# Kernel tuning notes

Measured on AMD Instinct MI355X. Metric: run time of the kernel, lower is better.

## Reference

```python
import jax, jax.numpy as jnp
import numpy as np

N = 100000   # nodes
E = 800000   # edges
D = 64       # hidden_channels
H = 4        # heads
C = D        # out_channels per head (PyG: out_channels=hidden)


def setup_inputs() -> dict:
    key = jax.random.key(0)
    ks = jax.random.split(key, 20)
    inp = {}
    inp['x'] = jax.random.normal(ks[0], (N, D), dtype=jnp.float32)
    inp['edge_index'] = jax.random.randint(ks[1], (2, E), 0, N, dtype=jnp.int32)
    i = 2
    for layer in (1, 2):
        for nm in ('Wq', 'Wk', 'Wv'):
            inp[f'{nm}{layer}'] = jax.random.normal(ks[i], (D, H * C), dtype=jnp.float32) * 0.05; i += 1
            inp[f'b{nm[1]}{layer}'] = jnp.zeros((H * C,), dtype=jnp.float32)
        inp[f'Ws{layer}'] = jax.random.normal(ks[i], (D, D), dtype=jnp.float32) * 0.05; i += 1
        inp[f'bs{layer}'] = jnp.zeros((D,), dtype=jnp.float32)
    return inp


def _transformer_conv(x, src, dst, Wq, bq, Wk, bk, Wv, bv, Ws, bs):
    n = x.shape[0]
    q = (x @ Wq + bq).reshape(n, H, C)
    k = (x @ Wk + bk).reshape(n, H, C)
    v = (x @ Wv + bv).reshape(n, H, C)
    # per-edge attention logits: [E, H]
    alpha = jnp.einsum('ehc,ehc->eh', q[dst], k[src]) / np.sqrt(C).astype(np.float32)
    # segment softmax over incoming edges of each destination node
    amax = jax.ops.segment_max(alpha, dst, num_segments=n)          # [N, H]
    ex = jnp.exp(alpha - amax[dst])                                 # [E, H]
    denom = jax.ops.segment_sum(ex, dst, num_segments=n)           # [N, H]
    attn = ex / (denom[dst] + 1e-16)                                # [E, H]
    msg = v[src] * attn[:, :, None]                                 # [E, H, C]
    agg = jax.ops.segment_sum(msg, dst, num_segments=n)            # [N, H, C]
    # concat=False -> mean over heads; root_weight skip connection
    return agg.mean(axis=1) + x @ Ws + bs


def reference(x, edge_index, Wq1, bq1, Wk1, bk1, Wv1, bv1, Ws1, bs1,
              Wq2, bq2, Wk2, bk2, Wv2, bv2, Ws2, bs2):
    src, dst = edge_index[0], edge_index[1]
    h = _transformer_conv(x, src, dst, Wq1, bq1, Wk1, bk1, Wv1, bv1, Ws1, bs1)
    h = jax.nn.relu(h)
    out = _transformer_conv(h, src, dst, Wq2, bq2, Wk2, bk2, Wv2, bv2, Ws2, bs2)
    return out
```

## Files before the change

kernel.cpp:

```cpp
#include <hip/hip_runtime.h>
#include <hip/hip_fp16.h>
#include <math.h>


typedef __attribute__((ext_vector_type(8))) short bf16x8;
typedef __attribute__((ext_vector_type(4))) float f32x4;
typedef __attribute__((ext_vector_type(2))) float f32x2;

#define QKSCALE 32.0f
#define C_EXP2 1.760325e-4f

__device__ inline unsigned short f2bf(float f) {
    unsigned int u = __float_as_uint(f);
    u = (u + 0x7fffu + ((u >> 16) & 1u)) >> 16;
    return (unsigned short)u;
}

#if __has_builtin(__builtin_amdgcn_cvt_pk_fp8_f32) && __has_builtin(__builtin_amdgcn_cvt_pk_f32_fp8)
#define HW_FP8 1
#endif

#ifndef HW_FP8
__device__ inline unsigned int fp8_enc1(float f) {
    unsigned int u = __float_as_uint(f);
    unsigned int s = (u >> 24) & 0x80u;
    float a = fabsf(f);
    if (a >= 448.f) return s | 0x7Eu;
    if (a < 0.015625f) return s;
    unsigned int ua = __float_as_uint(a);
    unsigned int r = ua + 0x7FFFFu + ((ua >> 20) & 1u);
    int e = (int)((r >> 23) & 255u) - 120;
    unsigned int m = (r >> 20) & 7u;
    if (e < 1) return s;
    if (e > 15) return s | 0x7Eu;
    return s | (unsigned int)((e << 3) | m);
}
__device__ inline float fp8_dec1(unsigned int b) {
    unsigned int e = (b >> 3) & 15u, m = b & 7u;
    float v;
    if (e) v = __uint_as_float(((e + 120u) << 23) | (m << 20));
    else   v = (float)m * 0.001953125f;
    return (b & 0x80u) ? -v : v;
}
#endif

__device__ inline unsigned int fp8x4_pack(float f0, float f1, float f2, float f3) {
#ifdef HW_FP8
    int pk = __builtin_amdgcn_cvt_pk_fp8_f32(f0, f1, 0, false);
    pk = __builtin_amdgcn_cvt_pk_fp8_f32(f2, f3, pk, true);
    return (unsigned int)pk;
#else
    return fp8_enc1(f0) | (fp8_enc1(f1) << 8) | (fp8_enc1(f2) << 16) | (fp8_enc1(f3) << 24);
#endif
}

__device__ inline float4 fp8x4_unpack(unsigned int k) {
#ifdef HW_FP8
    f32x2 lo = __builtin_amdgcn_cvt_pk_f32_fp8((int)k, false);
    f32x2 hi = __builtin_amdgcn_cvt_pk_f32_fp8((int)k, true);
    return make_float4(lo[0], lo[1], hi[0], hi[1]);
#else
    return make_float4(fp8_dec1(k & 255u), fp8_dec1((k >> 8) & 255u),
                       fp8_dec1((k >> 16) & 255u), fp8_dec1(k >> 24));
#endif
}

__device__ inline unsigned int i8x4_pack(float f0, float f1, float f2, float f3) {
    int a = (int)rintf(f0 * QKSCALE); a = a < -127 ? -127 : (a > 127 ? 127 : a);
    int b = (int)rintf(f1 * QKSCALE); b = b < -127 ? -127 : (b > 127 ? 127 : b);
    int c = (int)rintf(f2 * QKSCALE); c = c < -127 ? -127 : (c > 127 ? 127 : c);
    int d = (int)rintf(f3 * QKSCALE); d = d < -127 ? -127 : (d > 127 ? 127 : d);
    return (unsigned int)((a & 255) | ((b & 255) << 8) | ((c & 255) << 16) | ((d & 255) << 24));
}

__device__ inline int sdot4(unsigned int a, unsigned int b, int c) {
#if __has_builtin(__builtin_amdgcn_sdot4)
    return __builtin_amdgcn_sdot4((int)a, (int)b, c, false);
#else
    int r = c;
#pragma unroll
    for (int i = 0; i < 4; ++i) {
        int ai = (int)(a << (24 - 8 * i)) >> 24;
        int bi = (int)(b << (24 - 8 * i)) >> 24;
        r += ai * bi;
    }
    return r;
#endif
}

__global__ void k_setup(
    const float* __restrict__ x, unsigned short* __restrict__ Xb, int ncast4,
    const float* __restrict__ Wq1, const float* __restrict__ Wk1,
    const float* __restrict__ Wv1, const float* __restrict__ Ws1,
    const float* __restrict__ Wq2, const float* __restrict__ Wk2,
    const float* __restrict__ Wv2, const float* __restrict__ Ws2,
    unsigned short* __restrict__ Wt,
    int* __restrict__ counts, int N, int castBl)
{
    int b = blockIdx.x, tid = threadIdx.x;
    if (b < castBl) {
        int i = b * 256 + tid;
        if (i < ncast4) {
            float4 v = ((const float4*)x)[i];
            ushort4 o;
            o.x = f2bf(v.x); o.y = f2bf(v.y); o.z = f2bf(v.z); o.w = f2bf(v.w);
            ((ushort4*)Xb)[i] = o;
        }
    } else if (b < castBl + 416) {
        int j = (b - castBl) * 256 + tid;
        int layer = j / 53248;
        int r = j % 53248;
        if (r < 49152) {
            int m = r / 16384, w = r % 16384;
            int n = w / 64, k = w % 64;
            const float* W = (layer == 0)
                ? ((m == 0) ? Wq1 : (m == 1) ? Wk1 : Wv1)
                : ((m == 0) ? Wq2 : (m == 1) ? Wk2 : Wv2);
            Wt[layer * 53248 + m * 16384 + n * 64 + k] = f2bf(W[k * 256 + n]);
        } else {
            int w = r - 49152;
            int n = w / 64, k = w % 64;
            const float* W = (layer == 0) ? Ws1 : Ws2;
            Wt[layer * 53248 + 49152 + n * 64 + k] = f2bf(W[k * 64 + n]);
        }
    } else {
        int i = (b - castBl - 416) * 256 + tid;
        if (i < N) counts[i] = 0;
    }
}

#define SCAN_B 256
#define SCAN_CHUNK 2048
__global__ void k_scan1(const int* __restrict__ counts, int n,
                        int* __restrict__ offs, int* __restrict__ bsums) {
    __shared__ int lds[SCAN_B];
    int b = blockIdx.x, tid = threadIdx.x;
    int base = b * SCAN_CHUNK + tid * 8;
    int v[8]; int s = 0;
#pragma unroll
    for (int i = 0; i < 8; ++i) { int idx = base + i; int c = (idx < n) ? counts[idx] : 0; v[i] = s; s += c; }
    lds[tid] = s;
    for (int off = 1; off < SCAN_B; off <<= 1) {
        __syncthreads();
        int x = (tid >= off) ? lds[tid - off] : 0;
        __syncthreads();
        lds[tid] += x;
    }
    __syncthreads();
    int texcl = lds[tid] - s;
#pragma unroll
    for (int i = 0; i < 8; ++i) { int idx = base + i; if (idx < n) offs[idx] = texcl + v[i]; }
    if (tid == SCAN_B - 1) bsums[b] = lds[tid];
}

__global__ void k_scan2(int* bsums, int nb) {
    __shared__ int lds[256];
    int t = threadIdx.x;
    if (nb > 256) {
        if (t == 0) { int s = 0; for (int i = 0; i < nb; ++i) { int c = bsums[i]; bsums[i] = s; s += c; } }
        return;
    }
    int v = (t < nb) ? bsums[t] : 0;
    lds[t] = v;
    for (int off = 1; off < 256; off <<= 1) {
        __syncthreads();
        int x = (t >= off) ? lds[t - off] : 0;
        __syncthreads();
        lds[t] += x;
    }
    __syncthreads();
    if (t < nb) bsums[t] = lds[t] - v;
}

__global__ void k_scatter(const int* __restrict__ src, const int* __restrict__ dst, int E,
                          const int* __restrict__ offs, const int* __restrict__ bsums,
                          const int* __restrict__ rank, int* __restrict__ csr_src) {
    int e = blockIdx.x * 256 + threadIdx.x;
    if (e < E) {
        int d = dst[e];
        csr_src[offs[d] + bsums[d >> 11] + rank[e]] = src[e];
    }
}

#define GST 68
__global__ __launch_bounds__(256) void k_gemm(
    const unsigned short* __restrict__ Xb, int nrows,
    const unsigned short* __restrict__ WtL,
    const float* __restrict__ bqp, const float* __restrict__ bkp,
    const float* __restrict__ bvp, const float* __restrict__ bsp,
    unsigned char* __restrict__ Qb, unsigned char* __restrict__ KVb,
    unsigned char* __restrict__ Sb,
    const int* __restrict__ dstp, int histE,
    int* __restrict__ counts, int* __restrict__ rank, int gemmBl)
{
    __shared__ unsigned char st[4 * 64 * GST];
    int tid = threadIdx.x;
    if (blockIdx.x >= gemmBl) {
        int e = (blockIdx.x - gemmBl) * 256 + tid;
        if (e < histE) rank[e] = atomicAdd(&counts[dstp[e]], 1);
        return;
    }
    int wave = tid >> 6, lane = tid & 63;
    int quad = lane >> 4, n16 = lane & 15;
    int r0 = blockIdx.x * 64;
    unsigned char* wst = st + wave * 64 * GST;

    const unsigned short* Wq = WtL;
    const unsigned short* Wk = WtL + 16384;
    const unsigned short* Wv = WtL + 32768;
    const unsigned short* Ws = WtL + 49152;

    bf16x8 fQ[8], fK[8], fV[8], fS[2];
    float4 cQ[4], cK[4], cV[4], cS;
#pragma unroll
    for (int c = 0; c < 4; ++c) {
        int ct = wave * 4 + c;
        int roff = (ct * 16 + n16) * 64 + quad * 8;
        fQ[2 * c]     = *(const bf16x8*)(Wq + roff);
        fQ[2 * c + 1] = *(const bf16x8*)(Wq + roff + 32);
        fK[2 * c]     = *(const bf16x8*)(Wk + roff);
        fK[2 * c + 1] = *(const bf16x8*)(Wk + roff + 32);
        fV[2 * c]     = *(const bf16x8*)(Wv + roff);
        fV[2 * c + 1] = *(const bf16x8*)(Wv + roff + 32);
        cQ[c] = *(const float4*)(bqp + ct * 16 + quad * 4);
        cK[c] = *(const float4*)(bkp + ct * 16 + quad * 4);
        cV[c] = *(const float4*)(bvp + ct * 16 + quad * 4);
    }
    {
        int roff = (wave * 16 + n16) * 64 + quad * 8;
        fS[0] = *(const bf16x8*)(Ws + roff);
        fS[1] = *(const bf16x8*)(Ws + roff + 32);
        cS = *(const float4*)(bsp + wave * 16 + quad * 4);
    }
    bf16x8 a0[4], a1[4];
#pragma unroll
    for (int g = 0; g < 4; ++g) {
        int node = r0 + g * 16 + n16;
        int nodec = (node < nrows) ? node : (nrows - 1);
        a0[g] = *(const bf16x8*)(Xb + (size_t)nodec * 64 + quad * 8);
        a1[g] = *(const bf16x8*)(Xb + (size_t)nodec * 64 + 32 + quad * 8);
    }

    auto do_mat = [&](const bf16x8* fm, const float4* cm,
                      unsigned char* base, int stride, bool isInt8) {
#pragma unroll
        for (int g = 0; g < 4; ++g) {
#pragma unroll
            for (int c = 0; c < 4; ++c) {
                f32x4 acc = {0.f, 0.f, 0.f, 0.f};
                acc = __builtin_amdgcn_mfma_f32_16x16x32_bf16(fm[2 * c], a0[g], acc, 0, 0, 0);
                acc = __builtin_amdgcn_mfma_f32_16x16x32_bf16(fm[2 * c + 1], a1[g], acc, 0, 0, 0);
                float f0 = acc[0] + cm[c].x, f1 = acc[1] + cm[c].y;
                float f2 = acc[2] + cm[c].z, f3 = acc[3] + cm[c].w;
                unsigned int pk = isInt8 ? i8x4_pack(f0, f1, f2, f3)
                                         : fp8x4_pack(f0, f1, f2, f3);
                *(unsigned int*)(wst + (g * 16 + n16) * GST + c * 16 + quad * 4) = pk;
            }
        }
#pragma unroll
        for (int it = 0; it < 4; ++it) {
            int row = it * 16 + (lane >> 2);
            uint4 v = *(const uint4*)(wst + row * GST + (lane & 3) * 16);
            int node = r0 + row;
            if (node < nrows)
                *(uint4*)(base + (size_t)node * stride + wave * 64 + (lane & 3) * 16) = v;
        }
    };
    do_mat(fQ, cQ, Qb, 256, true);
    do_mat(fK, cK, KVb, 512, true);
    do_mat(fV, cV, KVb + 256, 512, false);
#pragma unroll
    for (int g = 0; g < 4; ++g) {
        f32x4 acc = {0.f, 0.f, 0.f, 0.f};
        acc = __builtin_amdgcn_mfma_f32_16x16x32_bf16(fS[0], a0[g], acc, 0, 0, 0);
        acc = __builtin_amdgcn_mfma_f32_16x16x32_bf16(fS[1], a1[g], acc, 0, 0, 0);
        *(float4*)(wst + (g * 16 + n16) * GST + quad * 16) =
            make_float4(acc[0] + cS.x, acc[1] + cS.y, acc[2] + cS.z, acc[3] + cS.w);
    }
#pragma unroll
    for (int it = 0; it < 4; ++it) {
        int row = it * 16 + (lane >> 2);
        uint4 v = *(const uint4*)(wst + row * GST + (lane & 3) * 16);
        int node = r0 + row;
        if (node < nrows)
            *(uint4*)(Sb + (size_t)node * 256 + wave * 64 + (lane & 3) * 16) = v;
    }
}

__global__ __launch_bounds__(256) void k_attn(
    const unsigned char* __restrict__ Qb, const unsigned char* __restrict__ KVb,
    const unsigned char* __restrict__ Sb,
    const int* __restrict__ offs, const int* __restrict__ bsums,
    const int* __restrict__ csr_src,
    float* __restrict__ out, unsigned short* __restrict__ Xb,
    int n, int Etot, int mode)
{
    int node = blockIdx.x * 4 + (threadIdx.x >> 6);
    if (node >= n) return;
    int lane = threadIdx.x & 63;
    int sl = lane & 31;
    int half = lane >> 5;
    uint2 q8 = *(const uint2*)(Qb + (size_t)node * 256 + sl * 8);
    int beg = offs[node] + bsums[node >> 11];
    int end = (node + 1 < n) ? (offs[node + 1] + bsums[(node + 1) >> 11]) : Etot;
    float l = 0.f;
    float acc[8];
#pragma unroll
    for (int i = 0; i < 8; ++i) acc[i] = 0.f;
    for (int base = beg; base < end; base += 8) {
        int cnt = end - base; if (cnt > 8) cnt = 8;
        int my = (lane < cnt) ? csr_src[base + lane] : 0;
        uint2 kk[4], vv[4];
#pragma unroll
        for (int p = 0; p < 4; ++p) {
            int idx = __shfl(my, 2 * p + half);
            const unsigned char* row = KVb + (size_t)idx * 512 + sl * 8;
            kk[p] = *(const uint2*)(row);
            vv[p] = *(const uint2*)(row + 256);
        }
#pragma unroll
        for (int p = 0; p < 4; ++p) {
            int d = sdot4(kk[p].x, q8.x, 0);
            d = sdot4(kk[p].y, q8.y, d);
            d += __shfl_xor(d, 1); d += __shfl_xor(d, 2); d += __shfl_xor(d, 4);
            float w = __builtin_exp2f((float)d * C_EXP2);
            w = (2 * p + half < cnt) ? w : 0.f;
            l += w;
            float4 va = fp8x4_unpack(vv[p].x);
            float4 vb = fp8x4_unpack(vv[p].y);
            acc[0] += va.x * w; acc[1] += va.y * w;
            acc[2] += va.z * w; acc[3] += va.w * w;
            acc[4] += vb.x * w; acc[5] += vb.y * w;
            acc[6] += vb.z * w; acc[7] += vb.w * w;
        }
    }
    l += __shfl_xor(l, 32);
#pragma unroll
    for (int i = 0; i < 8; ++i) acc[i] += __shfl_xor(acc[i], 32);
    float inv = 1.f / (l + 1e-16f);
#pragma unroll
    for (int i = 0; i < 8; ++i) acc[i] *= inv;
#pragma unroll
    for (int i = 0; i < 8; ++i) {
        acc[i] += __shfl_xor(acc[i], 8);
        acc[i] += __shfl_xor(acc[i], 16);
        acc[i] *= 0.25f;
    }
    if (lane < 8) {
        const float* Srow = (const float*)(Sb + (size_t)node * 256);
        float4 s0 = *(const float4*)(Srow + lane * 8);
        float4 s1 = *(const float4*)(Srow + lane * 8 + 4);
        float r0 = acc[0] + s0.x, r1 = acc[1] + s0.y;
        float r2 = acc[2] + s0.z, r3 = acc[3] + s0.w;
        float r4 = acc[4] + s1.x, r5 = acc[5] + s1.y;
        float r6 = acc[6] + s1.z, r7 = acc[7] + s1.w;
        if (mode == 1) {
            r0 = fmaxf(r0, 0.f); r1 = fmaxf(r1, 0.f);
            r2 = fmaxf(r2, 0.f); r3 = fmaxf(r3, 0.f);
            r4 = fmaxf(r4, 0.f); r5 = fmaxf(r5, 0.f);
            r6 = fmaxf(r6, 0.f); r7 = fmaxf(r7, 0.f);
            uint4 o;
            o.x = (unsigned int)f2bf(r0) | ((unsigned int)f2bf(r1) << 16);
            o.y = (unsigned int)f2bf(r2) | ((unsigned int)f2bf(r3) << 16);
            o.z = (unsigned int)f2bf(r4) | ((unsigned int)f2bf(r5) << 16);
            o.w = (unsigned int)f2bf(r6) | ((unsigned int)f2bf(r7) << 16);
            *(uint4*)(Xb + (size_t)node * 64 + lane * 8) = o;
        } else {
            *(float4*)(out + (size_t)node * 64 + lane * 8) = make_float4(r0, r1, r2, r3);
            *(float4*)(out + (size_t)node * 64 + lane * 8 + 4) = make_float4(r4, r5, r6, r7);
        }
    }
}

extern "C" void kernel_launch(void* const* d_in, const int* in_sizes, int n_in,
                              void* d_out, int out_size, void* d_ws, size_t ws_size,
                              hipStream_t stream)
{
    const float* x  = (const float*)d_in[0];
    const int*   ei = (const int*)d_in[1];
    int N = in_sizes[0] / 64;
    int E = in_sizes[1] / 2;
    const int* srcp = ei;
    const int* dstp = ei + E;
    const float* Wq1 = (const float*)d_in[2],  *bq1 = (const float*)d_in[3];
    const float* Wk1 = (const float*)d_in[4],  *bk1 = (const float*)d_in[5];
    const float* Wv1 = (const float*)d_in[6],  *bv1 = (const float*)d_in[7];
    const float* Ws1 = (const float*)d_in[8],  *bs1 = (const float*)d_in[9];
    const float* Wq2 = (const float*)d_in[10], *bq2 = (const float*)d_in[11];
    const float* Wk2 = (const float*)d_in[12], *bk2 = (const float*)d_in[13];
    const float* Wv2 = (const float*)d_in[14], *bv2 = (const float*)d_in[15];
    const float* Ws2 = (const float*)d_in[16], *bs2 = (const float*)d_in[17];
    float* out = (float*)d_out;

    char* ws = (char*)d_ws;
    size_t off = 0;
    auto alloc = [&](size_t bytes) -> void* {
        void* p = ws + off;
        off = (off + bytes + 255) & ~(size_t)255;
        return p;
    };
    unsigned short* Xb = (unsigned short*)alloc((size_t)N * 64 * 2);
    unsigned char* Qb  = (unsigned char*)alloc(((size_t)N + 64) * 256);
    unsigned char* KVb = (unsigned char*)alloc(((size_t)N + 64) * 512);
    unsigned char* Sb  = (unsigned char*)alloc(((size_t)N + 64) * 256);
    unsigned short* Wt = (unsigned short*)alloc(2 * 53248 * 2);
    int* counts = (int*)alloc((size_t)N * 4);
    int* rank   = (int*)alloc((size_t)E * 4);
    int* offs   = (int*)alloc((size_t)N * 4);
    int* bsums  = (int*)alloc(1024 * 4);
    int* csr    = (int*)alloc((size_t)E * 4);
    (void)n_in; (void)out_size;
    if (off > ws_size) return;

    int ebl = (E + 255) / 256;
    int nb_scan = (N + SCAN_CHUNK - 1) / SCAN_CHUNK;
    int row_bl = (N + 63) / 64;
    int attn_bl = (N + 3) / 4;
    int ncast4 = N * 16;
    int castBl = (ncast4 + 255) / 256;
    int zeroBl = (N + 255) / 256;

    k_setup<<<castBl + 416 + zeroBl, 256, 0, stream>>>(
        x, Xb, ncast4, Wq1, Wk1, Wv1, Ws1, Wq2, Wk2, Wv2, Ws2, Wt, counts, N, castBl);

    k_gemm<<<row_bl + ebl, 256, 0, stream>>>(
        Xb, N, Wt, bq1, bk1, bv1, bs1, Qb, KVb, Sb,
        dstp, E, counts, rank, row_bl);

    k_scan1<<<nb_scan, SCAN_B, 0, stream>>>(counts, N, offs, bsums);
    k_scan2<<<1, 256, 0, stream>>>(bsums, nb_scan);
    k_scatter<<<ebl, 256, 0, stream>>>(srcp, dstp, E, offs, bsums, rank, csr);

    k_attn<<<attn_bl, 256, 0, stream>>>(Qb, KVb, Sb, offs, bsums, csr, out, Xb, N, E, 1);

    k_gemm<<<row_bl, 256, 0, stream>>>(
        Xb, N, Wt + 53248, bq2, bk2, bv2, bs2, Qb, KVb, Sb,
        dstp, 0, counts, rank, row_bl);

    k_attn<<<attn_bl, 256, 0, stream>>>(Qb, KVb, Sb, offs, bsums, csr, out, Xb, N, E, 0);
}
```

Before: 405.3 us.

## Interleave per-node Q/K/V/S into one 1KB record and double-buffer GEMM staging

Merges the separate Q, KV and S buffers into one per-node 1024-byte record (Q, K, V, S at fixed offsets). The GEMM now stages full 64-row tiles across all waves in two LDS buffers and writes whole contiguous rows, so stores are more coalesced. Weight loading is now per matrix, which reduces register pressure and allows a launch_bounds occupancy hint of 4. The cost is block-wide syncs between stages, plus a wider 1KB stride for the gathered K/V rows in attention, which may hurt cache-line locality for those gathers.

```diff
diff --git a/kernel.cpp b/kernel.cpp
--- a/kernel.cpp
+++ b/kernel.cpp
@@ -182,18 +182,17 @@
     }
 }
 
-#define GST 68
-__global__ __launch_bounds__(256) void k_gemm(
+#define GROW 272
+__global__ __launch_bounds__(256, 4) void k_gemm(
     const unsigned short* __restrict__ Xb, int nrows,
     const unsigned short* __restrict__ WtL,
     const float* __restrict__ bqp, const float* __restrict__ bkp,
     const float* __restrict__ bvp, const float* __restrict__ bsp,
-    unsigned char* __restrict__ Qb, unsigned char* __restrict__ KVb,
-    unsigned char* __restrict__ Sb,
+    unsigned char* __restrict__ NB,
     const int* __restrict__ dstp, int histE,
     int* __restrict__ counts, int* __restrict__ rank, int gemmBl)
 {
-    __shared__ unsigned char st[4 * 64 * GST];
+    __shared__ unsigned char st[2][64 * GROW];
     int tid = threadIdx.x;
     if (blockIdx.x >= gemmBl) {
         int e = (blockIdx.x - gemmBl) * 256 + tid;
@@ -203,35 +202,7 @@
     int wave = tid >> 6, lane = tid & 63;
     int quad = lane >> 4, n16 = lane & 15;
     int r0 = blockIdx.x * 64;
-    unsigned char* wst = st + wave * 64 * GST;
-
-    const unsigned short* Wq = WtL;
-    const unsigned short* Wk = WtL + 16384;
-    const unsigned short* Wv = WtL + 32768;
-    const unsigned short* Ws = WtL + 49152;
-
-    bf16x8 fQ[8], fK[8], fV[8], fS[2];
-    float4 cQ[4], cK[4], cV[4], cS;
-#pragma unroll
-    for (int c = 0; c < 4; ++c) {
-        int ct = wave * 4 + c;
-        int roff = (ct * 16 + n16) * 64 + quad * 8;
-        fQ[2 * c]     = *(const bf16x8*)(Wq + roff);
-        fQ[2 * c + 1] = *(const bf16x8*)(Wq + roff + 32);
-        fK[2 * c]     = *(const bf16x8*)(Wk + roff);
-        fK[2 * c + 1] = *(const bf16x8*)(Wk + roff + 32);
-        fV[2 * c]     = *(const bf16x8*)(Wv + roff);
-        fV[2 * c + 1] = *(const bf16x8*)(Wv + roff + 32);
-        cQ[c] = *(const float4*)(bqp + ct * 16 + quad * 4);
-        cK[c] = *(const float4*)(bkp + ct * 16 + quad * 4);
-        cV[c] = *(const float4*)(bvp + ct * 16 + quad * 4);
-    }
-    {
-        int roff = (wave * 16 + n16) * 64 + quad * 8;
-        fS[0] = *(const bf16x8*)(Ws + roff);
-        fS[1] = *(const bf16x8*)(Ws + roff + 32);
-        cS = *(const float4*)(bsp + wave * 16 + quad * 4);
-    }
+
     bf16x8 a0[4], a1[4];
 #pragma unroll
     for (int g = 0; g < 4; ++g) {
@@ -241,55 +212,84 @@
         a1[g] = *(const bf16x8*)(Xb + (size_t)nodec * 64 + 32 + quad * 8);
     }
 
-    auto do_mat = [&](const bf16x8* fm, const float4* cm,
-                      unsigned char* base, int stride, bool isInt8) {
-#pragma unroll
-        for (int g = 0; g < 4; ++g) {
-#pragma unroll
-            for (int c = 0; c < 4; ++c) {
+    bf16x8 f[8]; float4 cb[4];
+    auto loadW = [&](const unsigned short* W, const float* bp) {
+#pragma unroll
+        for (int c = 0; c < 4; ++c) {
+            int roff = ((wave * 4 + c) * 16 + n16) * 64 + quad * 8;
+            f[2 * c]     = *(const bf16x8*)(W + roff);
+            f[2 * c + 1] = *(const bf16x8*)(W + roff + 32);
+            cb[c]        = *(const float4*)(bp + (wave * 4 + c) * 16 + quad * 4);
+        }
+    };
+    auto stage = [&](int buf, bool isInt8) {
+#pragma unroll
+        for (int c = 0; c < 4; ++c) {
+#pragma unroll
+            for (int g = 0; g < 4; ++g) {
                 f32x4 acc = {0.f, 0.f, 0.f, 0.f};
-                acc = __builtin_amdgcn_mfma_f32_16x16x32_bf16(fm[2 * c], a0[g], acc, 0, 0, 0);
-                acc = __builtin_amdgcn_mfma_f32_16x16x32_bf16(fm[2 * c + 1], a1[g], acc, 0, 0, 0);
-                float f0 = acc[0] + cm[c].x, f1 = acc[1] + cm[c].y;
-                float f2 = acc[2] + cm[c].z, f3 = acc[3] + cm[c].w;
+                acc = __builtin_amdgcn_mfma_f32_16x16x32_bf16(f[2 * c],     a0[g], acc, 0, 0, 0);
+                acc = __builtin_amdgcn_mfma_f32_16x16x32_bf16(f[2 * c + 1], a1[g], acc, 0, 0, 0);
+                float f0 = acc[0] + cb[c].x, f1 = acc[1] + cb[c].y;
+                float f2 = acc[2] + cb[c].z, f3 = acc[3] + cb[c].w;
                 unsigned int pk = isInt8 ? i8x4_pack(f0, f1, f2, f3)
                                          : fp8x4_pack(f0, f1, f2, f3);
-                *(unsigned int*)(wst + (g * 16 + n16) * GST + c * 16 + quad * 4) = pk;
+                *(unsigned int*)(st[buf] + (g * 16 + n16) * GROW + wave * 64 + c * 16 + quad * 4) = pk;
             }
         }
+    };
+    auto flush = [&](int buf, int matoff) {
 #pragma unroll
         for (int it = 0; it < 4; ++it) {
-            int row = it * 16 + (lane >> 2);
-            uint4 v = *(const uint4*)(wst + row * GST + (lane & 3) * 16);
-            int node = r0 + row;
+            int nl = wave * 16 + it * 4 + (lane >> 4);
+            uint4 v = *(const uint4*)(st[buf] + nl * GROW + (lane & 15) * 16);
+            int node = r0 + nl;
             if (node < nrows)
-                *(uint4*)(base + (size_t)node * stride + wave * 64 + (lane & 3) * 16) = v;
+                *(uint4*)(NB + (size_t)node * 1024 + matoff + (lane & 15) * 16) = v;
         }
     };
-    do_mat(fQ, cQ, Qb, 256, true);
-    do_mat(fK, cK, KVb, 512, true);
-    do_mat(fV, cV, KVb + 256, 512, false);
+
+    const unsigned short* Wq = WtL;
+    const unsigned short* Wk = WtL + 16384;
+    const unsigned short* Wv = WtL + 32768;
+    const unsigned short* Ws = WtL + 49152;
+
+    loadW(Wq, bqp);
+    stage(0, true);
+    __syncthreads();
+
+    loadW(Wk, bkp);
+    flush(0, 0);
+    stage(1, true);
+    __syncthreads();
+
+    loadW(Wv, bvp);
+    flush(1, 256);
+    stage(0, false);
+    __syncthreads();
+
+    bf16x8 s0, s1; float4 cs;
+    {
+        int roff = (wave * 16 + n16) * 64 + quad * 8;
+        s0 = *(const bf16x8*)(Ws + roff);
+        s1 = *(const bf16x8*)(Ws + roff + 32);
+        cs = *(const float4*)(bsp + wave * 16 + quad * 4);
+    }
+    flush(0, 512);
 #pragma unroll
     for (int g = 0; g < 4; ++g) {
         f32x4 acc = {0.f, 0.f, 0.f, 0.f};
-        acc = __builtin_amdgcn_mfma_f32_16x16x32_bf16(fS[0], a0[g], acc, 0, 0, 0);
-        acc = __builtin_amdgcn_mfma_f32_16x16x32_bf16(fS[1], a1[g], acc, 0, 0, 0);
-        *(float4*)(wst + (g * 16 + n16) * GST + quad * 16) =
-            make_float4(acc[0] + cS.x, acc[1] + cS.y, acc[2] + cS.z, acc[3] + cS.w);
-    }
-#pragma unroll
-    for (int it = 0; it < 4; ++it) {
-        int row = it * 16 + (lane >> 2);
-        uint4 v = *(const uint4*)(wst + row * GST + (lane & 3) * 16);
-        int node = r0 + row;
-        if (node < nrows)
-            *(uint4*)(Sb + (size_t)node * 256 + wave * 64 + (lane & 3) * 16) = v;
-    }
+        acc = __builtin_amdgcn_mfma_f32_16x16x32_bf16(s0, a0[g], acc, 0, 0, 0);
+        acc = __builtin_amdgcn_mfma_f32_16x16x32_bf16(s1, a1[g], acc, 0, 0, 0);
+        *(float4*)(st[1] + (g * 16 + n16) * GROW + wave * 64 + quad * 16) =
+            make_float4(acc[0] + cs.x, acc[1] + cs.y, acc[2] + cs.z, acc[3] + cs.w);
+    }
+    __syncthreads();
+    flush(1, 768);
 }
 
 __global__ __launch_bounds__(256) void k_attn(
-    const unsigned char* __restrict__ Qb, const unsigned char* __restrict__ KVb,
-    const unsigned char* __restrict__ Sb,
+    const unsigned char* __restrict__ NB,
     const int* __restrict__ offs, const int* __restrict__ bsums,
     const int* __restrict__ csr_src,
     float* __restrict__ out, unsigned short* __restrict__ Xb,
@@ -300,7 +300,7 @@
     int lane = threadIdx.x & 63;
     int sl = lane & 31;
     int half = lane >> 5;
-    uint2 q8 = *(const uint2*)(Qb + (size_t)node * 256 + sl * 8);
+    uint2 q8 = *(const uint2*)(NB + (size_t)node * 1024 + sl * 8);
     int beg = offs[node] + bsums[node >> 11];
     int end = (node + 1 < n) ? (offs[node + 1] + bsums[(node + 1) >> 11]) : Etot;
     float l = 0.f;
@@ -314,7 +314,7 @@
 #pragma unroll
         for (int p = 0; p < 4; ++p) {
             int idx = __shfl(my, 2 * p + half);
-            const unsigned char* row = KVb + (size_t)idx * 512 + sl * 8;
+            const unsigned char* row = NB + (size_t)idx * 1024 + 256 + sl * 8;
             kk[p] = *(const uint2*)(row);
             vv[p] = *(const uint2*)(row + 256);
         }
@@ -347,7 +347,7 @@
         acc[i] *= 0.25f;
     }
     if (lane < 8) {
-        const float* Srow = (const float*)(Sb + (size_t)node * 256);
+        const float* Srow = (const float*)(NB + (size_t)node * 1024 + 768);
         float4 s0 = *(const float4*)(Srow + lane * 8);
         float4 s1 = *(const float4*)(Srow + lane * 8 + 4);
         float r0 = acc[0] + s0.x, r1 = acc[1] + s0.y;
@@ -400,9 +400,7 @@
         return p;
     };
     unsigned short* Xb = (unsigned short*)alloc((size_t)N * 64 * 2);
-    unsigned char* Qb  = (unsigned char*)alloc(((size_t)N + 64) * 256);
-    unsigned char* KVb = (unsigned char*)alloc(((size_t)N + 64) * 512);
-    unsigned char* Sb  = (unsigned char*)alloc(((size_t)N + 64) * 256);
+    unsigned char* NB  = (unsigned char*)alloc(((size_t)N + 64) * 1024);
     unsigned short* Wt = (unsigned short*)alloc(2 * 53248 * 2);
     int* counts = (int*)alloc((size_t)N * 4);
     int* rank   = (int*)alloc((size_t)E * 4);
@@ -424,18 +422,18 @@
         x, Xb, ncast4, Wq1, Wk1, Wv1, Ws1, Wq2, Wk2, Wv2, Ws2, Wt, counts, N, castBl);
 
     k_gemm<<<row_bl + ebl, 256, 0, stream>>>(
-        Xb, N, Wt, bq1, bk1, bv1, bs1, Qb, KVb, Sb,
+        Xb, N, Wt, bq1, bk1, bv1, bs1, NB,
         dstp, E, counts, rank, row_bl);
 
     k_scan1<<<nb_scan, SCAN_B, 0, stream>>>(counts, N, offs, bsums);
     k_scan2<<<1, 256, 0, stream>>>(bsums, nb_scan);
     k_scatter<<<ebl, 256, 0, stream>>>(srcp, dstp, E, offs, bsums, rank, csr);
 
-    k_attn<<<attn_bl, 256, 0, stream>>>(Qb, KVb, Sb, offs, bsums, csr, out, Xb, N, E, 1);
+    k_attn<<<attn_bl, 256, 0, stream>>>(NB, offs, bsums, csr, out, Xb, N, E, 1);
 
     k_gemm<<<row_bl, 256, 0, stream>>>(
-        Xb, N, Wt + 53248, bq2, bk2, bv2, bs2, Qb, KVb, Sb,
+        Xb, N, Wt + 53248, bq2, bk2, bv2, bs2, NB,
         dstp, 0, counts, rank, row_bl);
 
-    k_attn<<<attn_bl, 256, 0, stream>>>(Qb, KVb, Sb, offs, bsums, csr, out, Xb, N, E, 0);
-}
+    k_attn<<<attn_bl, 256, 0, stream>>>(NB, offs, bsums, csr, out, Xb, N, E, 0);
+}
```

New measurement: 384.6 us. 1.05x faster.

## Make GEMM persistent with prefetch and interleave Q/K/V/S per node row

Applied to the files above, without the earlier changes.

The projection GEMM becomes a persistent kernel capped at 512 blocks. Each block keeps its weight fragments in registers, loops over 64-row tiles and prefetches the next tile's activations while computing the current one. Biases are staged in shared memory and used as the initial MFMA accumulator. The Q, KV and S buffers are merged into one 1024-byte record per node, so the attention kernel reads Q, K, V and S from a single contiguous row. The aim is to amortise weight loads, overlap input loads with compute and improve locality of the gathers, at the cost of higher register pressure and a larger per-row stride when reading K/V.

```diff
diff --git a/kernel.cpp b/kernel.cpp
--- a/kernel.cpp
+++ b/kernel.cpp
@@ -183,77 +183,81 @@
 }
 
 #define GST 68
-__global__ __launch_bounds__(256) void k_gemm(
+__global__ __launch_bounds__(256, 2) void k_gemm(
     const unsigned short* __restrict__ Xb, int nrows,
     const unsigned short* __restrict__ WtL,
     const float* __restrict__ bqp, const float* __restrict__ bkp,
     const float* __restrict__ bvp, const float* __restrict__ bsp,
-    unsigned char* __restrict__ Qb, unsigned char* __restrict__ KVb,
-    unsigned char* __restrict__ Sb,
+    unsigned char* __restrict__ NB,
     const int* __restrict__ dstp, int histE,
-    int* __restrict__ counts, int* __restrict__ rank, int gemmBl)
+    int* __restrict__ counts, int* __restrict__ rank, int gemmBl, int ntiles)
 {
-    __shared__ unsigned char st[4 * 64 * GST];
+    __shared__ unsigned char st[4][64 * GST];
+    __shared__ float bias[832];
     int tid = threadIdx.x;
     if (blockIdx.x >= gemmBl) {
         int e = (blockIdx.x - gemmBl) * 256 + tid;
         if (e < histE) rank[e] = atomicAdd(&counts[dstp[e]], 1);
         return;
     }
-    int wave = tid >> 6, lane = tid & 63;
+    int qtr = tid >> 6, lane = tid & 63;
     int quad = lane >> 4, n16 = lane & 15;
-    int r0 = blockIdx.x * 64;
-    unsigned char* wst = st + wave * 64 * GST;
+    unsigned char* wst = st[qtr];
+
+    if (tid < 208) {
+        float4 b4;
+        if (tid < 64)       b4 = ((const float4*)bqp)[tid];
+        else if (tid < 128) b4 = ((const float4*)bkp)[tid - 64];
+        else if (tid < 192) b4 = ((const float4*)bvp)[tid - 128];
+        else                b4 = ((const float4*)bsp)[tid - 192];
+        ((float4*)bias)[tid] = b4;
+    }
 
     const unsigned short* Wq = WtL;
     const unsigned short* Wk = WtL + 16384;
     const unsigned short* Wv = WtL + 32768;
     const unsigned short* Ws = WtL + 49152;
-
     bf16x8 fQ[8], fK[8], fV[8], fS[2];
-    float4 cQ[4], cK[4], cV[4], cS;
 #pragma unroll
     for (int c = 0; c < 4; ++c) {
-        int ct = wave * 4 + c;
-        int roff = (ct * 16 + n16) * 64 + quad * 8;
+        int roff = ((qtr * 4 + c) * 16 + n16) * 64 + quad * 8;
         fQ[2 * c]     = *(const bf16x8*)(Wq + roff);
         fQ[2 * c + 1] = *(const bf16x8*)(Wq + roff + 32);
         fK[2 * c]     = *(const bf16x8*)(Wk + roff);
         fK[2 * c + 1] = *(const bf16x8*)(Wk + roff + 32);
         fV[2 * c]     = *(const bf16x8*)(Wv + roff);
         fV[2 * c + 1] = *(const bf16x8*)(Wv + roff + 32);
-        cQ[c] = *(const float4*)(bqp + ct * 16 + quad * 4);
-        cK[c] = *(const float4*)(bkp + ct * 16 + quad * 4);
-        cV[c] = *(const float4*)(bvp + ct * 16 + quad * 4);
     }
     {
-        int roff = (wave * 16 + n16) * 64 + quad * 8;
+        int roff = (qtr * 16 + n16) * 64 + quad * 8;
         fS[0] = *(const bf16x8*)(Ws + roff);
         fS[1] = *(const bf16x8*)(Ws + roff + 32);
-        cS = *(const float4*)(bsp + wave * 16 + quad * 4);
-    }
-    bf16x8 a0[4], a1[4];
-#pragma unroll
-    for (int g = 0; g < 4; ++g) {
-        int node = r0 + g * 16 + n16;
-        int nodec = (node < nrows) ? node : (nrows - 1);
-        a0[g] = *(const bf16x8*)(Xb + (size_t)nodec * 64 + quad * 8);
-        a1[g] = *(const bf16x8*)(Xb + (size_t)nodec * 64 + 32 + quad * 8);
-    }
-
-    auto do_mat = [&](const bf16x8* fm, const float4* cm,
-                      unsigned char* base, int stride, bool isInt8) {
+    }
+    __syncthreads();
+
+    auto loadA = [&](int t, bf16x8 (&x0)[4], bf16x8 (&x1)[4]) {
+        int r0 = t * 64;
 #pragma unroll
         for (int g = 0; g < 4; ++g) {
-#pragma unroll
-            for (int c = 0; c < 4; ++c) {
-                f32x4 acc = {0.f, 0.f, 0.f, 0.f};
-                acc = __builtin_amdgcn_mfma_f32_16x16x32_bf16(fm[2 * c], a0[g], acc, 0, 0, 0);
-                acc = __builtin_amdgcn_mfma_f32_16x16x32_bf16(fm[2 * c + 1], a1[g], acc, 0, 0, 0);
-                float f0 = acc[0] + cm[c].x, f1 = acc[1] + cm[c].y;
-                float f2 = acc[2] + cm[c].z, f3 = acc[3] + cm[c].w;
-                unsigned int pk = isInt8 ? i8x4_pack(f0, f1, f2, f3)
-                                         : fp8x4_pack(f0, f1, f2, f3);
+            int node = r0 + g * 16 + n16;
+            int nodec = (node < nrows) ? node : (nrows - 1);
+            x0[g] = *(const bf16x8*)(Xb + (size_t)nodec * 64 + quad * 8);
+            x1[g] = *(const bf16x8*)(Xb + (size_t)nodec * 64 + 32 + quad * 8);
+        }
+    };
+
+    auto do_mat = [&](const bf16x8 (&fm)[8], int boff, int matoff, bool isInt8,
+                      int r0, const bf16x8 (&x0)[4], const bf16x8 (&x1)[4]) {
+#pragma unroll
+        for (int c = 0; c < 4; ++c) {
+            float4 cb = *(const float4*)(bias + boff + qtr * 64 + c * 16 + quad * 4);
+#pragma unroll
+            for (int g = 0; g < 4; ++g) {
+                f32x4 acc = {cb.x, cb.y, cb.z, cb.w};
+                acc = __builtin_amdgcn_mfma_f32_16x16x32_bf16(fm[2 * c],     x0[g], acc, 0, 0, 0);
+                acc = __builtin_amdgcn_mfma_f32_16x16x32_bf16(fm[2 * c + 1], x1[g], acc, 0, 0, 0);
+                unsigned int pk = isInt8 ? i8x4_pack(acc[0], acc[1], acc[2], acc[3])
+                                         : fp8x4_pack(acc[0], acc[1], acc[2], acc[3]);
                 *(unsigned int*)(wst + (g * 16 + n16) * GST + c * 16 + quad * 4) = pk;
             }
         }
@@ -261,35 +265,48 @@
         for (int it = 0; it < 4; ++it) {
             int row = it * 16 + (lane >> 2);
             uint4 v = *(const uint4*)(wst + row * GST + (lane & 3) * 16);
-            int node = r0 + row;
-            if (node < nrows)
-                *(uint4*)(base + (size_t)node * stride + wave * 64 + (lane & 3) * 16) = v;
+            int nd = r0 + row;
+            if (nd < nrows)
+                *(uint4*)(NB + (size_t)nd * 1024 + matoff + qtr * 64 + (lane & 3) * 16) = v;
         }
     };
-    do_mat(fQ, cQ, Qb, 256, true);
-    do_mat(fK, cK, KVb, 512, true);
-    do_mat(fV, cV, KVb + 256, 512, false);
-#pragma unroll
-    for (int g = 0; g < 4; ++g) {
-        f32x4 acc = {0.f, 0.f, 0.f, 0.f};
-        acc = __builtin_amdgcn_mfma_f32_16x16x32_bf16(fS[0], a0[g], acc, 0, 0, 0);
-        acc = __builtin_amdgcn_mfma_f32_16x16x32_bf16(fS[1], a1[g], acc, 0, 0, 0);
-        *(float4*)(wst + (g * 16 + n16) * GST + quad * 16) =
-            make_float4(acc[0] + cS.x, acc[1] + cS.y, acc[2] + cS.z, acc[3] + cS.w);
-    }
-#pragma unroll
-    for (int it = 0; it < 4; ++it) {
-        int row = it * 16 + (lane >> 2);
-        uint4 v = *(const uint4*)(wst + row * GST + (lane & 3) * 16);
-        int node = r0 + row;
-        if (node < nrows)
-            *(uint4*)(Sb + (size_t)node * 256 + wave * 64 + (lane & 3) * 16) = v;
+
+    bf16x8 a0[4], a1[4], b0[4], b1[4];
+    int t = blockIdx.x;
+    if (t < ntiles) loadA(t, a0, a1);
+    for (; t < ntiles; t += gemmBl) {
+        int tn = t + gemmBl;
+        if (tn < ntiles) loadA(tn, b0, b1);
+        int r0 = t * 64;
+        do_mat(fQ, 0,   0,   true,  r0, a0, a1);
+        do_mat(fK, 256, 256, true,  r0, a0, a1);
+        do_mat(fV, 512, 512, false, r0, a0, a1);
+        {
+            float4 cs = *(const float4*)(bias + 768 + qtr * 16 + quad * 4);
+#pragma unroll
+            for (int g = 0; g < 4; ++g) {
+                f32x4 acc = {cs.x, cs.y, cs.z, cs.w};
+                acc = __builtin_amdgcn_mfma_f32_16x16x32_bf16(fS[0], a0[g], acc, 0, 0, 0);
+                acc = __builtin_amdgcn_mfma_f32_16x16x32_bf16(fS[1], a1[g], acc, 0, 0, 0);
+                *(float4*)(wst + (g * 16 + n16) * GST + quad * 16) =
+                    make_float4(acc[0], acc[1], acc[2], acc[3]);
+            }
+#pragma unroll
+            for (int it = 0; it < 4; ++it) {
+                int row = it * 16 + (lane >> 2);
+                uint4 v = *(const uint4*)(wst + row * GST + (lane & 3) * 16);
+                int nd = r0 + row;
+                if (nd < nrows)
+                    *(uint4*)(NB + (size_t)nd * 1024 + 768 + qtr * 64 + (lane & 3) * 16) = v;
+            }
+        }
+#pragma unroll
+        for (int g = 0; g < 4; ++g) { a0[g] = b0[g]; a1[g] = b1[g]; }
     }
 }
 
 __global__ __launch_bounds__(256) void k_attn(
-    const unsigned char* __restrict__ Qb, const unsigned char* __restrict__ KVb,
-    const unsigned char* __restrict__ Sb,
+    const unsigned char* __restrict__ NB,
     const int* __restrict__ offs, const int* __restrict__ bsums,
     const int* __restrict__ csr_src,
     float* __restrict__ out, unsigned short* __restrict__ Xb,
@@ -300,7 +317,7 @@
     int lane = threadIdx.x & 63;
     int sl = lane & 31;
     int half = lane >> 5;
-    uint2 q8 = *(const uint2*)(Qb + (size_t)node * 256 + sl * 8);
+    uint2 q8 = *(const uint2*)(NB + (size_t)node * 1024 + sl * 8);
     int beg = offs[node] + bsums[node >> 11];
     int end = (node + 1 < n) ? (offs[node + 1] + bsums[(node + 1) >> 11]) : Etot;
     float l = 0.f;
@@ -314,7 +331,7 @@
 #pragma unroll
         for (int p = 0; p < 4; ++p) {
             int idx = __shfl(my, 2 * p + half);
-            const unsigned char* row = KVb + (size_t)idx * 512 + sl * 8;
+            const unsigned char* row = NB + (size_t)idx * 1024 + 256 + sl * 8;
             kk[p] = *(const uint2*)(row);
             vv[p] = *(const uint2*)(row + 256);
         }
@@ -347,7 +364,7 @@
         acc[i] *= 0.25f;
     }
     if (lane < 8) {
-        const float* Srow = (const float*)(Sb + (size_t)node * 256);
+        const float* Srow = (const float*)(NB + (size_t)node * 1024 + 768);
         float4 s0 = *(const float4*)(Srow + lane * 8);
         float4 s1 = *(const float4*)(Srow + lane * 8 + 4);
         float r0 = acc[0] + s0.x, r1 = acc[1] + s0.y;
@@ -400,9 +417,7 @@
         return p;
     };
     unsigned short* Xb = (unsigned short*)alloc((size_t)N * 64 * 2);
-    unsigned char* Qb  = (unsigned char*)alloc(((size_t)N + 64) * 256);
-    unsigned char* KVb = (unsigned char*)alloc(((size_t)N + 64) * 512);
-    unsigned char* Sb  = (unsigned char*)alloc(((size_t)N + 64) * 256);
+    unsigned char* NB  = (unsigned char*)alloc(((size_t)N + 64) * 1024);
     unsigned short* Wt = (unsigned short*)alloc(2 * 53248 * 2);
     int* counts = (int*)alloc((size_t)N * 4);
     int* rank   = (int*)alloc((size_t)E * 4);
@@ -414,7 +429,9 @@
 
     int ebl = (E + 255) / 256;
     int nb_scan = (N + SCAN_CHUNK - 1) / SCAN_CHUNK;
-    int row_bl = (N + 63) / 64;
+    int ntiles = (N + 63) / 64;
+    int gemm_bl = ntiles < 512 ? ntiles : 512;
+    int hist_bl = (E + 255) / 256;
     int attn_bl = (N + 3) / 4;
     int ncast4 = N * 16;
     int castBl = (ncast4 + 255) / 256;
@@ -423,19 +440,19 @@
     k_setup<<<castBl + 416 + zeroBl, 256, 0, stream>>>(
         x, Xb, ncast4, Wq1, Wk1, Wv1, Ws1, Wq2, Wk2, Wv2, Ws2, Wt, counts, N, castBl);
 
-    k_gemm<<<row_bl + ebl, 256, 0, stream>>>(
-        Xb, N, Wt, bq1, bk1, bv1, bs1, Qb, KVb, Sb,
-        dstp, E, counts, rank, row_bl);
+    k_gemm<<<gemm_bl + hist_bl, 256, 0, stream>>>(
+        Xb, N, Wt, bq1, bk1, bv1, bs1, NB,
+        dstp, E, counts, rank, gemm_bl, ntiles);
 
     k_scan1<<<nb_scan, SCAN_B, 0, stream>>>(counts, N, offs, bsums);
     k_scan2<<<1, 256, 0, stream>>>(bsums, nb_scan);
     k_scatter<<<ebl, 256, 0, stream>>>(srcp, dstp, E, offs, bsums, rank, csr);
 
-    k_attn<<<attn_bl, 256, 0, stream>>>(Qb, KVb, Sb, offs, bsums, csr, out, Xb, N, E, 1);
-
-    k_gemm<<<row_bl, 256, 0, stream>>>(
-        Xb, N, Wt + 53248, bq2, bk2, bv2, bs2, Qb, KVb, Sb,
-        dstp, 0, counts, rank, row_bl);
-
-    k_attn<<<attn_bl, 256, 0, stream>>>(Qb, KVb, Sb, offs, bsums, csr, out, Xb, N, E, 0);
-}
+    k_attn<<<attn_bl, 256, 0, stream>>>(NB, offs, bsums, csr, out, Xb, N, E, 1);
+
+    k_gemm<<<gemm_bl, 256, 0, stream>>>(
+        Xb, N, Wt + 53248, bq2, bk2, bv2, bs2, NB,
+        dstp, 0, counts, rank, gemm_bl, ntiles);
+
+    k_attn<<<attn_bl, 256, 0, stream>>>(NB, offs, bsums, csr, out, Xb, N, E, 0);
+}
```

New measurement: 366.6 us. 9.5% less time.
